# Kernel optimization log

Measured on AMD Instinct MI355X. Metric: run time of the kernel, lower is better.

The kernel has to match this reference:

```python
import jax, jax.numpy as jnp
import numpy as np

N_HEAD, D_K, D_V, D_MODEL, D_O = 8, 64, 64, 512, 512
B, S = 2, 4096

def setup_inputs() -> dict:
    key = jax.random.key(0)
    ks = jax.random.split(key, 11)
    s = 1.0 / np.sqrt(D_MODEL)
    so = 1.0 / np.sqrt(N_HEAD * D_V)
    return {
        'q': jax.random.normal(ks[0], (B, S, D_MODEL), jnp.float32),
        'k': jax.random.normal(ks[1], (B, S, D_MODEL), jnp.float32),
        'v': jax.random.normal(ks[2], (B, S, D_MODEL), jnp.float32),
        'Wq': jax.random.uniform(ks[3], (D_MODEL, N_HEAD * D_K), jnp.float32, -s, s),
        'bq': jax.random.uniform(ks[4], (N_HEAD * D_K,), jnp.float32, -s, s),
        'Wk': jax.random.uniform(ks[5], (D_MODEL, N_HEAD * D_K), jnp.float32, -s, s),
        'bk': jax.random.uniform(ks[6], (N_HEAD * D_K,), jnp.float32, -s, s),
        'Wv': jax.random.uniform(ks[7], (D_MODEL, N_HEAD * D_V), jnp.float32, -s, s),
        'bv': jax.random.uniform(ks[8], (N_HEAD * D_V,), jnp.float32, -s, s),
        'Wo': jax.random.uniform(ks[9], (N_HEAD * D_V, D_O), jnp.float32, -so, so),
        'bo': jax.random.uniform(ks[10], (D_O,), jnp.float32, -so, so),
    }

def reference(q, k, v, Wq, bq, Wk, bk, Wv, bv, Wo, bo):
    b, nq, _ = q.shape
    nk = k.shape[1]
    scale = jnp.asarray(np.power(D_K, 0.5), q.dtype)
    # project and split heads: [b, s, h, d]
    qh = (q @ Wq + bq).reshape(b, nq, N_HEAD, D_K)
    kh = (k @ Wk + bk).reshape(b, nk, N_HEAD, D_K)
    vh = (v @ Wv + bv).reshape(b, nk, N_HEAD, D_V)
    # scaled dot-product attention (full score matrix, as in original)
    scores = jnp.einsum('bqhd,bkhd->bhqk', qh, kh) / scale
    attn = jax.nn.softmax(scores, axis=-1)
    out = jnp.einsum('bhqk,bkhd->bqhd', attn, vh)
    # concat heads (head-major over d_v, matching the original view) and output proj
    out = out.reshape(b, nq, N_HEAD * D_V)
    return out @ Wo + bo
```

## Files before the change

kernel.cpp:

```cpp
#include <hip/hip_runtime.h>
#include <hip/hip_bf16.h>

#define NHEAD 8
#define DK_ 64
#define DM_ 512
#define S_LEN 4096
#define NTOK 8192

typedef __bf16 bf16x8 __attribute__((ext_vector_type(8)));
typedef float f32x4 __attribute__((ext_vector_type(4)));
typedef float f32x16 __attribute__((ext_vector_type(16)));
typedef unsigned int uint4v __attribute__((ext_vector_type(4)));

__device__ __forceinline__ unsigned short f2bf(float f) {
    union { float f; unsigned u; } x; x.f = f;
    unsigned u = x.u;
    u += 0x7FFFu + ((u >> 16) & 1u);
    return (unsigned short)(u >> 16);
}

#if __has_builtin(__builtin_amdgcn_cvt_pk_bf16_f32)
__device__ __forceinline__ unsigned int pkbf(float a, float b) {
    auto r = __builtin_amdgcn_cvt_pk_bf16_f32(a, b);
    unsigned int u; __builtin_memcpy(&u, &r, 4); return u;
}
#else
__device__ __forceinline__ unsigned int pkbf(float a, float b) {
    return (unsigned)f2bf(a) | ((unsigned)f2bf(b) << 16);
}
#endif

#if __has_builtin(__builtin_amdgcn_exp2f)
#define EXP2F(x) __builtin_amdgcn_exp2f(x)
#else
#define EXP2F(x) exp2f(x)
#endif

#if __has_builtin(__builtin_amdgcn_permlane32_swap)
__device__ __forceinline__ void pl32swap(unsigned int& a, unsigned int& b) {
    auto r = __builtin_amdgcn_permlane32_swap(a, b, false, false);
    a = r[0]; b = r[1];
}
#else
__device__ __forceinline__ void pl32swap(unsigned int& a, unsigned int& b) {
    int lane = threadIdx.x & 63;
    unsigned int ax = __shfl_xor((int)a, 32, 64);
    unsigned int bx = __shfl_xor((int)b, 32, 64);
    unsigned int na = (lane < 32) ? a : bx;
    unsigned int nb = (lane < 32) ? ax : b;
    a = na; b = nb;
}
#endif

#define GLOAD_LDS16(gptr, ldsbase) \
    __builtin_amdgcn_global_load_lds((const __attribute__((address_space(1))) unsigned int*)(gptr), \
                                     (__attribute__((address_space(3))) unsigned int*)(ldsbase), 16, 0, 0)

__global__ __launch_bounds__(256) void xcvt(const float* __restrict__ q, const float* __restrict__ k,
                                            const float* __restrict__ v, unsigned short* __restrict__ Xbf) {
    int z = blockIdx.y;
    const float* X = (z == 0) ? q : (z == 1) ? k : v;
    size_t off = (size_t)blockIdx.x * 1024 + threadIdx.x * 4;
    float4 val = *(const float4*)&X[off];
    uint2 o; o.x = pkbf(val.x, val.y); o.y = pkbf(val.z, val.w);
    *(uint2*)&Xbf[(size_t)z * NTOK * DM_ + off] = o;
}

__global__ __launch_bounds__(256) void wtrans(const float* __restrict__ Wq, const float* __restrict__ Wk,
                                              const float* __restrict__ Wv, const float* __restrict__ Wo,
                                              unsigned short* __restrict__ Wt) {
    int z = blockIdx.z;
    const float* W = (z == 0) ? Wq : (z == 1) ? Wk : (z == 2) ? Wv : Wo;
    unsigned short* out = Wt + (size_t)z * DM_ * DM_;
    __shared__ float t[64][65];
    int bn = blockIdx.x * 64, bk = blockIdx.y * 64;
    int tid = threadIdx.x;
    int r0 = tid >> 4, c4 = (tid & 15) * 4;
#pragma unroll
    for (int i = 0; i < 4; i++) {
        int r = r0 + i * 16;
        float4 v = *(const float4*)&W[(size_t)(bk + r) * DM_ + bn + c4];
        t[r][c4] = v.x; t[r][c4 + 1] = v.y; t[r][c4 + 2] = v.z; t[r][c4 + 3] = v.w;
    }
    __syncthreads();
    int n0 = tid >> 4, k4 = (tid & 15) * 4;
#pragma unroll
    for (int i = 0; i < 4; i++) {
        int n = n0 + i * 16;
        ushort4 o;
        o.x = f2bf(t[k4 + 0][n]); o.y = f2bf(t[k4 + 1][n]);
        o.z = f2bf(t[k4 + 2][n]); o.w = f2bf(t[k4 + 3][n]);
        *(ushort4*)&out[(size_t)(bn + n) * DM_ + bk + k4] = o;
    }
}

__device__ __forceinline__ void proj_epilogue(int z, f32x4 (&acc)[4][4], const float* bias,
                                              unsigned short* out, float scale,
                                              int m0, int n0, int mb, int nb, int ln, int qd) {
    float bvv[4];
#pragma unroll
    for (int nt = 0; nt < 4; nt++) bvv[nt] = bias[n0 + nb + nt * 16 + ln];
#pragma unroll
    for (int mt = 0; mt < 4; mt++) {
        int mrow0 = m0 + mb + mt * 16 + qd * 4;
        int b = mrow0 >> 12, s = mrow0 & 4095;
#pragma unroll
        for (int nt = 0; nt < 4; nt++) {
            int ncol = n0 + nb + nt * 16 + ln;
            int h = ncol >> 6, d = ncol & 63;
            if (z == 2) {
                uint2 o;
                o.x = pkbf((acc[mt][nt][0] + bvv[nt]) * scale, (acc[mt][nt][1] + bvv[nt]) * scale);
                o.y = pkbf((acc[mt][nt][2] + bvv[nt]) * scale, (acc[mt][nt][3] + bvv[nt]) * scale);
                *(uint2*)&out[((size_t)(b * NHEAD + h) * DK_ + d) * S_LEN + s] = o;
            } else {
#pragma unroll
                for (int r = 0; r < 4; r++)
                    out[((size_t)(b * NHEAD + h) * S_LEN + (s + r)) * DK_ + d] =
                        f2bf((acc[mt][nt][r] + bvv[nt]) * scale);
            }
        }
    }
}

__global__ __launch_bounds__(256, 3) void qkv_bf(const unsigned short* __restrict__ Xbf,
                                                 const unsigned short* __restrict__ Wt,
                                                 const float* __restrict__ bq, const float* __restrict__ bk,
                                                 const float* __restrict__ bv,
                                                 unsigned short* __restrict__ Qh, unsigned short* __restrict__ Kh,
                                                 unsigned short* __restrict__ VhT) {
    int z = blockIdx.z;
    const unsigned short* X = Xbf + (size_t)z * NTOK * DM_;
    const unsigned short* W = Wt + (size_t)z * DM_ * DM_;
    const float* bias = (z == 0) ? bq : (z == 1) ? bk : bv;
    unsigned short* out = (z == 0) ? Qh : (z == 1) ? Kh : VhT;
    float scale = (z == 0) ? 0.125f * 1.44269504f : 1.0f;

    __shared__ unsigned short As[128 * 40];
    __shared__ unsigned short Bs[128 * 40];
    int tid = threadIdx.x;
    int n0 = blockIdx.x * 128, m0 = blockIdx.y * 128;
    int w = tid >> 6, lane = tid & 63;
    int ln = lane & 15, qd = lane >> 4;
    int mb = (w >> 1) * 64, nb = (w & 1) * 64;

    f32x4 acc[4][4];
#pragma unroll
    for (int i = 0; i < 4; i++)
#pragma unroll
        for (int j = 0; j < 4; j++) { f32x4 zz = {0.f, 0.f, 0.f, 0.f}; acc[i][j] = zz; }

    for (int kk = 0; kk < DM_; kk += 32) {
        __syncthreads();
#pragma unroll
        for (int i = 0; i < 2; i++) {
            int idx = i * 256 + tid;
            int row = idx >> 2, k8 = (idx & 3) * 8;
            uint4 va = *(const uint4*)&X[(size_t)(m0 + row) * DM_ + kk + k8];
            *(uint4*)&As[row * 40 + k8] = va;
            uint4 vb = *(const uint4*)&W[(size_t)(n0 + row) * DM_ + kk + k8];
            *(uint4*)&Bs[row * 40 + k8] = vb;
        }
        __syncthreads();
        bf16x8 af[4], bf[4];
#pragma unroll
        for (int mt = 0; mt < 4; mt++) af[mt] = *(const bf16x8*)&As[(mb + mt * 16 + ln) * 40 + qd * 8];
#pragma unroll
        for (int nt = 0; nt < 4; nt++) bf[nt] = *(const bf16x8*)&Bs[(nb + nt * 16 + ln) * 40 + qd * 8];
#pragma unroll
        for (int mt = 0; mt < 4; mt++)
#pragma unroll
            for (int nt = 0; nt < 4; nt++)
                acc[mt][nt] = __builtin_amdgcn_mfma_f32_16x16x32_bf16(af[mt], bf[nt], acc[mt][nt], 0, 0, 0);
    }
    proj_epilogue(z, acc, bias, out, scale, m0, n0, mb, nb, ln, qd);
}

__global__ __launch_bounds__(256, 3) void qkv_proj(const float* __restrict__ xq, const float* __restrict__ xk,
                                                   const float* __restrict__ xv, const unsigned short* __restrict__ Wt,
                                                   const float* __restrict__ bq, const float* __restrict__ bk,
                                                   const float* __restrict__ bv,
                                                   unsigned short* __restrict__ Qh, unsigned short* __restrict__ Kh,
                                                   unsigned short* __restrict__ VhT) {
    int z = blockIdx.z;
    const float* X = (z == 0) ? xq : (z == 1) ? xk : xv;
    const unsigned short* W = Wt + (size_t)z * DM_ * DM_;
    const float* bias = (z == 0) ? bq : (z == 1) ? bk : bv;
    unsigned short* out = (z == 0) ? Qh : (z == 1) ? Kh : VhT;
    float scale = (z == 0) ? 0.125f * 1.44269504f : 1.0f;

    __shared__ unsigned short As[128 * 40];
    __shared__ unsigned short Bs[128 * 40];
    int tid = threadIdx.x;
    int n0 = blockIdx.x * 128, m0 = blockIdx.y * 128;
    int w = tid >> 6, lane = tid & 63;
    int ln = lane & 15, qd = lane >> 4;
    int mb = (w >> 1) * 64, nb = (w & 1) * 64;

    f32x4 acc[4][4];
#pragma unroll
    for (int i = 0; i < 4; i++)
#pragma unroll
        for (int j = 0; j < 4; j++) { f32x4 zz = {0.f, 0.f, 0.f, 0.f}; acc[i][j] = zz; }

    for (int kk = 0; kk < DM_; kk += 32) {
        __syncthreads();
#pragma unroll
        for (int i = 0; i < 4; i++) {
            int idx = i * 256 + tid;
            int row = idx >> 3, k4 = (idx & 7) * 4;
            float4 v = *(const float4*)&X[(size_t)(m0 + row) * DM_ + kk + k4];
            uint2 o; o.x = pkbf(v.x, v.y); o.y = pkbf(v.z, v.w);
            *(uint2*)&As[row * 40 + k4] = o;
        }
#pragma unroll
        for (int i = 0; i < 2; i++) {
            int idx = i * 256 + tid;
            int row = idx >> 2, k8 = (idx & 3) * 8;
            uint4 v = *(const uint4*)&W[(size_t)(n0 + row) * DM_ + kk + k8];
            *(uint4*)&Bs[row * 40 + k8] = v;
        }
        __syncthreads();
        bf16x8 af[4], bf[4];
#pragma unroll
        for (int mt = 0; mt < 4; mt++) af[mt] = *(const bf16x8*)&As[(mb + mt * 16 + ln) * 40 + qd * 8];
#pragma unroll
        for (int nt = 0; nt < 4; nt++) bf[nt] = *(const bf16x8*)&Bs[(nb + nt * 16 + ln) * 40 + qd * 8];
#pragma unroll
        for (int mt = 0; mt < 4; mt++)
#pragma unroll
            for (int nt = 0; nt < 4; nt++)
                acc[mt][nt] = __builtin_amdgcn_mfma_f32_16x16x32_bf16(af[mt], bf[nt], acc[mt][nt], 0, 0, 0);
    }
    proj_epilogue(z, acc, bias, out, scale, m0, n0, mb, nb, ln, qd);
}

__global__ __launch_bounds__(256, 2) void flash_attn(const unsigned short* __restrict__ Qh,
                                                     const unsigned short* __restrict__ Kh,
                                                     const unsigned short* __restrict__ VhT,
                                                     unsigned short* __restrict__ Ao) {
    __shared__ unsigned short Ks[2][64 * 64];
    __shared__ unsigned short Vs[2][64 * 64];
    int i = blockIdx.x;
    int bh = (i & 7) + 8 * ((i >> 3) & 1);
    int qb = i >> 4;
    int tid = threadIdx.x;
    int w = tid >> 6, lane = tid & 63;
    int ln = lane & 31, hf = lane >> 5;
    int swz = ln & 7;
    int q0 = qb * 128 + w * 32;
    const unsigned short* Qp = Qh + (size_t)bh * S_LEN * DK_;
    const unsigned short* Kp = Kh + (size_t)bh * S_LEN * DK_;
    const unsigned short* Vp = VhT + (size_t)bh * DK_ * S_LEN;

    int sr = lane >> 3;
    int sc = (lane & 7) ^ sr;
    const unsigned short* ksrc = Kp + (size_t)(w * 16 + sr) * DK_ + sc * 8;
    const unsigned short* vsrc = Vp + (size_t)(w * 16 + sr) * S_LEN + sc * 8;

    bf16x8 qf[4];
#pragma unroll
    for (int s = 0; s < 4; s++)
        qf[s] = *(const bf16x8*)&Qp[(size_t)(q0 + ln) * DK_ + s * 16 + hf * 8];

    f32x16 oacc[2];
    { f32x16 z = {0.f}; oacc[0] = z; oacc[1] = z; }
    float lsum = 0.f;

    GLOAD_LDS16(ksrc, &Ks[0][w * 1024]);
    GLOAD_LDS16(ksrc + (size_t)8 * DK_, &Ks[0][w * 1024 + 512]);
    GLOAD_LDS16(vsrc, &Vs[0][w * 1024]);
    GLOAD_LDS16(vsrc + (size_t)8 * S_LEN, &Vs[0][w * 1024 + 512]);

    int p = 0;
    for (int ks = 0; ks < S_LEN; ks += 64, p ^= 1) {
        __syncthreads();
        if (ks + 64 < S_LEN) {
            const unsigned short* kn = ksrc + (size_t)(ks + 64) * DK_;
            const unsigned short* vn = vsrc + (ks + 64);
            GLOAD_LDS16(kn, &Ks[p ^ 1][w * 1024]);
            GLOAD_LDS16(kn + (size_t)8 * DK_, &Ks[p ^ 1][w * 1024 + 512]);
            GLOAD_LDS16(vn, &Vs[p ^ 1][w * 1024]);
            GLOAD_LDS16(vn + (size_t)8 * S_LEN, &Vs[p ^ 1][w * 1024 + 512]);
        }
        const unsigned short* KsT = &Ks[p][0];
        const unsigned short* VsT = &Vs[p][0];

#pragma unroll
        for (int kb = 0; kb < 2; kb++) {
            f32x16 st = {0.f};
#pragma unroll
            for (int s = 0; s < 4; s++) {
                bf16x8 kf = *(const bf16x8*)&KsT[(kb * 32 + ln) * 64 + ((2 * s + hf) ^ swz) * 8];
                st = __builtin_amdgcn_mfma_f32_32x32x16_bf16(kf, qf[s], st, 0, 0, 0);
            }
            float e[16];
#pragma unroll
            for (int r = 0; r < 16; r++) e[r] = EXP2F(st[r]);
            lsum += ((e[0] + e[1]) + (e[2] + e[3])) + ((e[4] + e[5]) + (e[6] + e[7]))
                  + ((e[8] + e[9]) + (e[10] + e[11])) + ((e[12] + e[13]) + (e[14] + e[15]));
            unsigned int g[8];
#pragma unroll
            for (int gi = 0; gi < 8; gi++) g[gi] = pkbf(e[2 * gi], e[2 * gi + 1]);
            pl32swap(g[0], g[2]); pl32swap(g[1], g[3]);
            pl32swap(g[4], g[6]); pl32swap(g[5], g[7]);
            bf16x8 b0, b1;
            { uint4v t = {g[0], g[1], g[2], g[3]}; __builtin_memcpy(&b0, &t, 16); }
            { uint4v t = {g[4], g[5], g[6], g[7]}; __builtin_memcpy(&b1, &t, 16); }
#pragma unroll
            for (int dt = 0; dt < 2; dt++) {
                int s0 = kb * 2;
                bf16x8 vf0 = *(const bf16x8*)&VsT[(dt * 32 + ln) * 64 + ((2 * s0 + hf) ^ swz) * 8];
                bf16x8 vf1 = *(const bf16x8*)&VsT[(dt * 32 + ln) * 64 + ((2 * s0 + 2 + hf) ^ swz) * 8];
                oacc[dt] = __builtin_amdgcn_mfma_f32_32x32x16_bf16(vf0, b0, oacc[dt], 0, 0, 0);
                oacc[dt] = __builtin_amdgcn_mfma_f32_32x32x16_bf16(vf1, b1, oacc[dt], 0, 0, 0);
            }
        }
    }

    float ltot = lsum + __shfl_xor(lsum, 32, 64);
    float inv = 1.0f / ltot;

    int bb = bh >> 3, hh = bh & 7;
    int token = bb * S_LEN + q0 + ln;
#pragma unroll
    for (int dt = 0; dt < 2; dt++)
#pragma unroll
        for (int gi = 0; gi < 8; gi++) {
            int d = dt * 32 + 2 * (gi & 1) + 8 * (gi >> 1) + 4 * hf;
            unsigned int o = pkbf(oacc[dt][2 * gi] * inv, oacc[dt][2 * gi + 1] * inv);
            *(unsigned int*)&Ao[(size_t)token * DM_ + hh * DK_ + d] = o;
        }
}

__global__ __launch_bounds__(256) void out_gemm(const unsigned short* __restrict__ A,
                                                const unsigned short* __restrict__ Wt,
                                                const float* __restrict__ bias, float* __restrict__ out) {
    __shared__ unsigned short As[128 * 40];
    __shared__ unsigned short Bs[128 * 40];
    int tid = threadIdx.x;
    int n0 = blockIdx.x * 128, m0 = blockIdx.y * 128;
    int w = tid >> 6, lane = tid & 63;
    int ln = lane & 15, qd = lane >> 4;
    int mb = (w >> 1) * 64, nb = (w & 1) * 64;

    f32x4 acc[4][4];
#pragma unroll
    for (int i = 0; i < 4; i++)
#pragma unroll
        for (int j = 0; j < 4; j++) { f32x4 z = {0.f, 0.f, 0.f, 0.f}; acc[i][j] = z; }

    for (int kk = 0; kk < DM_; kk += 32) {
        __syncthreads();
#pragma unroll
        for (int i = 0; i < 2; i++) {
            int idx = i * 256 + tid;
            int row = idx >> 2, k8 = (idx & 3) * 8;
            uint4 va = *(const uint4*)&A[(size_t)(m0 + row) * DM_ + kk + k8];
            *(uint4*)&As[row * 40 + k8] = va;
            uint4 vb = *(const uint4*)&Wt[(size_t)(n0 + row) * DM_ + kk + k8];
            *(uint4*)&Bs[row * 40 + k8] = vb;
        }
        __syncthreads();
        bf16x8 af[4], bf[4];
#pragma unroll
        for (int mt = 0; mt < 4; mt++) af[mt] = *(const bf16x8*)&As[(mb + mt * 16 + ln) * 40 + qd * 8];
#pragma unroll
        for (int nt = 0; nt < 4; nt++) bf[nt] = *(const bf16x8*)&Bs[(nb + nt * 16 + ln) * 40 + qd * 8];
#pragma unroll
        for (int mt = 0; mt < 4; mt++)
#pragma unroll
            for (int nt = 0; nt < 4; nt++)
                acc[mt][nt] = __builtin_amdgcn_mfma_f32_16x16x32_bf16(af[mt], bf[nt], acc[mt][nt], 0, 0, 0);
    }

    float bv[4];
#pragma unroll
    for (int nt = 0; nt < 4; nt++) bv[nt] = bias[n0 + nb + nt * 16 + ln];
#pragma unroll
    for (int mt = 0; mt < 4; mt++) {
        int mrow0 = m0 + mb + mt * 16 + qd * 4;
#pragma unroll
        for (int nt = 0; nt < 4; nt++) {
            int ncol = n0 + nb + nt * 16 + ln;
#pragma unroll
            for (int r = 0; r < 4; r++)
                out[(size_t)(mrow0 + r) * DM_ + ncol] = acc[mt][nt][r] + bv[nt];
        }
    }
}

extern "C" void kernel_launch(void* const* d_in, const int* in_sizes, int n_in,
                              void* d_out, int out_size, void* d_ws, size_t ws_size,
                              hipStream_t stream) {
    const float* q  = (const float*)d_in[0];
    const float* k  = (const float*)d_in[1];
    const float* v  = (const float*)d_in[2];
    const float* Wq = (const float*)d_in[3];
    const float* bq = (const float*)d_in[4];
    const float* Wk = (const float*)d_in[5];
    const float* bk = (const float*)d_in[6];
    const float* Wv = (const float*)d_in[7];
    const float* bv = (const float*)d_in[8];
    const float* Wo = (const float*)d_in[9];
    const float* bo = (const float*)d_in[10];
    float* out = (float*)d_out;

    unsigned short* Wt  = (unsigned short*)d_ws;
    unsigned short* Qh  = Wt + (size_t)4 * DM_ * DM_;
    unsigned short* Kh  = Qh + (size_t)NTOK * DM_;
    unsigned short* VhT = Kh + (size_t)NTOK * DM_;
    unsigned short* tail = VhT + (size_t)NTOK * DM_;

    size_t need_bf = ((size_t)4 * DM_ * DM_ + (size_t)6 * NTOK * DM_) * 2;

    wtrans<<<dim3(8, 8, 4), 256, 0, stream>>>(Wq, Wk, Wv, Wo, Wt);
    unsigned short* Ao = tail;
    if (ws_size >= need_bf) {
        unsigned short* Xbf = tail;
        xcvt<<<dim3(4096, 3), 256, 0, stream>>>(q, k, v, Xbf);
        qkv_bf<<<dim3(4, 64, 3), 256, 0, stream>>>(Xbf, Wt, bq, bk, bv, Qh, Kh, VhT);
    } else {
        qkv_proj<<<dim3(4, 64, 3), 256, 0, stream>>>(q, k, v, Wt, bq, bk, bv, Qh, Kh, VhT);
    }
    flash_attn<<<dim3(512), 256, 0, stream>>>(Qh, Kh, VhT, Ao);
    out_gemm<<<dim3(4, 64), 256, 0, stream>>>(Ao, Wt + (size_t)3 * DM_ * DM_, bo, out);
}
```

Measured before the change: 237.7 us.

## Merge prep kernels and use direct-to-LDS swizzled loads in projection GEMMs

```diff
diff --git a/kernel.cpp b/kernel.cpp
--- a/kernel.cpp
+++ b/kernel.cpp
@@ -36,61 +36,52 @@
 #define EXP2F(x) exp2f(x)
 #endif
 
-#if __has_builtin(__builtin_amdgcn_permlane32_swap)
 __device__ __forceinline__ void pl32swap(unsigned int& a, unsigned int& b) {
-    auto r = __builtin_amdgcn_permlane32_swap(a, b, false, false);
-    a = r[0]; b = r[1];
-}
-#else
-__device__ __forceinline__ void pl32swap(unsigned int& a, unsigned int& b) {
-    int lane = threadIdx.x & 63;
-    unsigned int ax = __shfl_xor((int)a, 32, 64);
-    unsigned int bx = __shfl_xor((int)b, 32, 64);
-    unsigned int na = (lane < 32) ? a : bx;
-    unsigned int nb = (lane < 32) ? ax : b;
-    a = na; b = nb;
-}
-#endif
+    asm volatile("v_permlane32_swap_b32 %0, %1" : "+v"(a), "+v"(b));
+}
 
 #define GLOAD_LDS16(gptr, ldsbase) \
     __builtin_amdgcn_global_load_lds((const __attribute__((address_space(1))) unsigned int*)(gptr), \
                                      (__attribute__((address_space(3))) unsigned int*)(ldsbase), 16, 0, 0)
 
-__global__ __launch_bounds__(256) void xcvt(const float* __restrict__ q, const float* __restrict__ k,
-                                            const float* __restrict__ v, unsigned short* __restrict__ Xbf) {
-    int z = blockIdx.y;
-    const float* X = (z == 0) ? q : (z == 1) ? k : v;
-    size_t off = (size_t)blockIdx.x * 1024 + threadIdx.x * 4;
-    float4 val = *(const float4*)&X[off];
-    uint2 o; o.x = pkbf(val.x, val.y); o.y = pkbf(val.z, val.w);
-    *(uint2*)&Xbf[(size_t)z * NTOK * DM_ + off] = o;
-}
-
-__global__ __launch_bounds__(256) void wtrans(const float* __restrict__ Wq, const float* __restrict__ Wk,
-                                              const float* __restrict__ Wv, const float* __restrict__ Wo,
-                                              unsigned short* __restrict__ Wt) {
-    int z = blockIdx.z;
-    const float* W = (z == 0) ? Wq : (z == 1) ? Wk : (z == 2) ? Wv : Wo;
-    unsigned short* out = Wt + (size_t)z * DM_ * DM_;
-    __shared__ float t[64][65];
-    int bn = blockIdx.x * 64, bk = blockIdx.y * 64;
+__global__ __launch_bounds__(256) void prep(const float* __restrict__ q, const float* __restrict__ k,
+                                            const float* __restrict__ v,
+                                            const float* __restrict__ Wq, const float* __restrict__ Wk,
+                                            const float* __restrict__ Wv, const float* __restrict__ Wo,
+                                            unsigned short* __restrict__ Wt, unsigned short* __restrict__ Xbf) {
+    int bid = blockIdx.x;
     int tid = threadIdx.x;
-    int r0 = tid >> 4, c4 = (tid & 15) * 4;
-#pragma unroll
-    for (int i = 0; i < 4; i++) {
-        int r = r0 + i * 16;
-        float4 v = *(const float4*)&W[(size_t)(bk + r) * DM_ + bn + c4];
-        t[r][c4] = v.x; t[r][c4 + 1] = v.y; t[r][c4 + 2] = v.z; t[r][c4 + 3] = v.w;
-    }
-    __syncthreads();
-    int n0 = tid >> 4, k4 = (tid & 15) * 4;
-#pragma unroll
-    for (int i = 0; i < 4; i++) {
-        int n = n0 + i * 16;
-        ushort4 o;
-        o.x = f2bf(t[k4 + 0][n]); o.y = f2bf(t[k4 + 1][n]);
-        o.z = f2bf(t[k4 + 2][n]); o.w = f2bf(t[k4 + 3][n]);
-        *(ushort4*)&out[(size_t)(bn + n) * DM_ + bk + k4] = o;
+    if (bid < 256) {
+        int z = bid >> 6, rem = bid & 63;
+        const float* W = (z == 0) ? Wq : (z == 1) ? Wk : (z == 2) ? Wv : Wo;
+        unsigned short* out = Wt + (size_t)z * DM_ * DM_;
+        __shared__ float t[64][65];
+        int bn = (rem & 7) * 64, bk = (rem >> 3) * 64;
+        int r0 = tid >> 4, c4 = (tid & 15) * 4;
+#pragma unroll
+        for (int i = 0; i < 4; i++) {
+            int r = r0 + i * 16;
+            float4 val = *(const float4*)&W[(size_t)(bk + r) * DM_ + bn + c4];
+            t[r][c4] = val.x; t[r][c4 + 1] = val.y; t[r][c4 + 2] = val.z; t[r][c4 + 3] = val.w;
+        }
+        __syncthreads();
+        int n0 = tid >> 4, k4 = (tid & 15) * 4;
+#pragma unroll
+        for (int i = 0; i < 4; i++) {
+            int n = n0 + i * 16;
+            ushort4 o;
+            o.x = f2bf(t[k4 + 0][n]); o.y = f2bf(t[k4 + 1][n]);
+            o.z = f2bf(t[k4 + 2][n]); o.w = f2bf(t[k4 + 3][n]);
+            *(ushort4*)&out[(size_t)(bn + n) * DM_ + bk + k4] = o;
+        }
+    } else {
+        int tt = bid - 256;
+        int z = tt >> 12, xb = tt & 4095;
+        const float* X = (z == 0) ? q : (z == 1) ? k : v;
+        size_t off = (size_t)xb * 1024 + tid * 4;
+        float4 val = *(const float4*)&X[off];
+        uint2 o; o.x = pkbf(val.x, val.y); o.y = pkbf(val.z, val.w);
+        *(uint2*)&Xbf[(size_t)z * NTOK * DM_ + off] = o;
     }
 }
 
@@ -123,12 +114,59 @@
     }
 }
 
-__global__ __launch_bounds__(256, 3) void qkv_bf(const unsigned short* __restrict__ Xbf,
-                                                 const unsigned short* __restrict__ Wt,
-                                                 const float* __restrict__ bq, const float* __restrict__ bk,
-                                                 const float* __restrict__ bv,
-                                                 unsigned short* __restrict__ Qh, unsigned short* __restrict__ Kh,
-                                                 unsigned short* __restrict__ VhT) {
+__device__ __forceinline__ void gemm_core(const unsigned short* __restrict__ A,
+                                          const unsigned short* __restrict__ B,
+                                          unsigned short* As, unsigned short* Bs,
+                                          int m0, int n0, f32x4 (&acc)[4][4]) {
+    int tid = threadIdx.x;
+    int w = tid >> 6, lane = tid & 63;
+    int ln = lane & 15, qd = lane >> 4;
+    int mb = (w >> 1) * 64, nb = (w & 1) * 64;
+    int sr = lane >> 3;
+    int sc8 = (lane & 7) ^ sr;
+    const unsigned short* asrc = A + (size_t)(m0 + w * 32 + sr) * DM_ + sc8 * 8;
+    const unsigned short* bsrc = B + (size_t)(n0 + w * 32 + sr) * DM_ + sc8 * 8;
+    unsigned short* adst = As + w * 32 * 64;
+    unsigned short* bdst = Bs + w * 32 * 64;
+
+    for (int kk = 0; kk < DM_; kk += 64) {
+        __syncthreads();
+#pragma unroll
+        for (int j = 0; j < 4; j++) {
+            GLOAD_LDS16(asrc + kk + (size_t)(j * 8) * DM_, adst + j * 8 * 64);
+            GLOAD_LDS16(bsrc + kk + (size_t)(j * 8) * DM_, bdst + j * 8 * 64);
+        }
+        __syncthreads();
+#pragma unroll
+        for (int k2 = 0; k2 < 2; k2++) {
+            bf16x8 af[4], bf[4];
+#pragma unroll
+            for (int mt = 0; mt < 4; mt++) {
+                int m = mb + mt * 16 + ln;
+                af[mt] = *(const bf16x8*)&As[m * 64 + ((k2 * 4 + qd) ^ (m & 7)) * 8];
+            }
+#pragma unroll
+            for (int nt = 0; nt < 4; nt++) {
+                int n = nb + nt * 16 + ln;
+                bf[nt] = *(const bf16x8*)&Bs[n * 64 + ((k2 * 4 + qd) ^ (n & 7)) * 8];
+            }
+#pragma unroll
+            for (int mt = 0; mt < 4; mt++)
+#pragma unroll
+                for (int nt = 0; nt < 4; nt++)
+                    acc[mt][nt] = __builtin_amdgcn_mfma_f32_16x16x32_bf16(af[mt], bf[nt], acc[mt][nt], 0, 0, 0);
+        }
+    }
+}
+
+__global__ __launch_bounds__(256) void qkv_bf(const unsigned short* __restrict__ Xbf,
+                                              const unsigned short* __restrict__ Wt,
+                                              const float* __restrict__ bq, const float* __restrict__ bk,
+                                              const float* __restrict__ bv,
+                                              unsigned short* __restrict__ Qh, unsigned short* __restrict__ Kh,
+                                              unsigned short* __restrict__ VhT) {
+    __shared__ unsigned short As[128 * 64];
+    __shared__ unsigned short Bs[128 * 64];
     int z = blockIdx.z;
     const unsigned short* X = Xbf + (size_t)z * NTOK * DM_;
     const unsigned short* W = Wt + (size_t)z * DM_ * DM_;
@@ -136,44 +174,17 @@
     unsigned short* out = (z == 0) ? Qh : (z == 1) ? Kh : VhT;
     float scale = (z == 0) ? 0.125f * 1.44269504f : 1.0f;
 
-    __shared__ unsigned short As[128 * 40];
-    __shared__ unsigned short Bs[128 * 40];
-    int tid = threadIdx.x;
     int n0 = blockIdx.x * 128, m0 = blockIdx.y * 128;
-    int w = tid >> 6, lane = tid & 63;
-    int ln = lane & 15, qd = lane >> 4;
-    int mb = (w >> 1) * 64, nb = (w & 1) * 64;
-
     f32x4 acc[4][4];
 #pragma unroll
     for (int i = 0; i < 4; i++)
 #pragma unroll
         for (int j = 0; j < 4; j++) { f32x4 zz = {0.f, 0.f, 0.f, 0.f}; acc[i][j] = zz; }
 
-    for (int kk = 0; kk < DM_; kk += 32) {
-        __syncthreads();
-#pragma unroll
-        for (int i = 0; i < 2; i++) {
-            int idx = i * 256 + tid;
-            int row = idx >> 2, k8 = (idx & 3) * 8;
-            uint4 va = *(const uint4*)&X[(size_t)(m0 + row) * DM_ + kk + k8];
-            *(uint4*)&As[row * 40 + k8] = va;
-            uint4 vb = *(const uint4*)&W[(size_t)(n0 + row) * DM_ + kk + k8];
-            *(uint4*)&Bs[row * 40 + k8] = vb;
-        }
-        __syncthreads();
-        bf16x8 af[4], bf[4];
-#pragma unroll
-        for (int mt = 0; mt < 4; mt++) af[mt] = *(const bf16x8*)&As[(mb + mt * 16 + ln) * 40 + qd * 8];
-#pragma unroll
-        for (int nt = 0; nt < 4; nt++) bf[nt] = *(const bf16x8*)&Bs[(nb + nt * 16 + ln) * 40 + qd * 8];
-#pragma unroll
-        for (int mt = 0; mt < 4; mt++)
-#pragma unroll
-            for (int nt = 0; nt < 4; nt++)
-                acc[mt][nt] = __builtin_amdgcn_mfma_f32_16x16x32_bf16(af[mt], bf[nt], acc[mt][nt], 0, 0, 0);
-    }
-    proj_epilogue(z, acc, bias, out, scale, m0, n0, mb, nb, ln, qd);
+    gemm_core(X, W, As, Bs, m0, n0, acc);
+
+    int lane = threadIdx.x & 63, w = threadIdx.x >> 6;
+    proj_epilogue(z, acc, bias, out, scale, m0, n0, (w >> 1) * 64, (w & 1) * 64, lane & 15, lane >> 4);
 }
 
 __global__ __launch_bounds__(256, 3) void qkv_proj(const float* __restrict__ xq, const float* __restrict__ xk,
@@ -209,16 +220,16 @@
         for (int i = 0; i < 4; i++) {
             int idx = i * 256 + tid;
             int row = idx >> 3, k4 = (idx & 7) * 4;
-            float4 v = *(const float4*)&X[(size_t)(m0 + row) * DM_ + kk + k4];
-            uint2 o; o.x = pkbf(v.x, v.y); o.y = pkbf(v.z, v.w);
+            float4 val = *(const float4*)&X[(size_t)(m0 + row) * DM_ + kk + k4];
+            uint2 o; o.x = pkbf(val.x, val.y); o.y = pkbf(val.z, val.w);
             *(uint2*)&As[row * 40 + k4] = o;
         }
 #pragma unroll
         for (int i = 0; i < 2; i++) {
             int idx = i * 256 + tid;
             int row = idx >> 2, k8 = (idx & 3) * 8;
-            uint4 v = *(const uint4*)&W[(size_t)(n0 + row) * DM_ + kk + k8];
-            *(uint4*)&Bs[row * 40 + k8] = v;
+            uint4 val = *(const uint4*)&W[(size_t)(n0 + row) * DM_ + kk + k8];
+            *(uint4*)&Bs[row * 40 + k8] = val;
         }
         __syncthreads();
         bf16x8 af[4], bf[4];
@@ -336,44 +347,21 @@
 __global__ __launch_bounds__(256) void out_gemm(const unsigned short* __restrict__ A,
                                                 const unsigned short* __restrict__ Wt,
                                                 const float* __restrict__ bias, float* __restrict__ out) {
-    __shared__ unsigned short As[128 * 40];
-    __shared__ unsigned short Bs[128 * 40];
+    __shared__ unsigned short As[128 * 64];
+    __shared__ unsigned short Bs[128 * 64];
+    int n0 = blockIdx.x * 128, m0 = blockIdx.y * 128;
+    f32x4 acc[4][4];
+#pragma unroll
+    for (int i = 0; i < 4; i++)
+#pragma unroll
+        for (int j = 0; j < 4; j++) { f32x4 z = {0.f, 0.f, 0.f, 0.f}; acc[i][j] = z; }
+
+    gemm_core(A, Wt, As, Bs, m0, n0, acc);
+
     int tid = threadIdx.x;
-    int n0 = blockIdx.x * 128, m0 = blockIdx.y * 128;
     int w = tid >> 6, lane = tid & 63;
     int ln = lane & 15, qd = lane >> 4;
     int mb = (w >> 1) * 64, nb = (w & 1) * 64;
-
-    f32x4 acc[4][4];
-#pragma unroll
-    for (int i = 0; i < 4; i++)
-#pragma unroll
-        for (int j = 0; j < 4; j++) { f32x4 z = {0.f, 0.f, 0.f, 0.f}; acc[i][j] = z; }
-
-    for (int kk = 0; kk < DM_; kk += 32) {
-        __syncthreads();
-#pragma unroll
-        for (int i = 0; i < 2; i++) {
-            int idx = i * 256 + tid;
-            int row = idx >> 2, k8 = (idx & 3) * 8;
-            uint4 va = *(const uint4*)&A[(size_t)(m0 + row) * DM_ + kk + k8];
-            *(uint4*)&As[row * 40 + k8] = va;
-            uint4 vb = *(const uint4*)&Wt[(size_t)(n0 + row) * DM_ + kk + k8];
-            *(uint4*)&Bs[row * 40 + k8] = vb;
-        }
-        __syncthreads();
-        bf16x8 af[4], bf[4];
-#pragma unroll
-        for (int mt = 0; mt < 4; mt++) af[mt] = *(const bf16x8*)&As[(mb + mt * 16 + ln) * 40 + qd * 8];
-#pragma unroll
-        for (int nt = 0; nt < 4; nt++) bf[nt] = *(const bf16x8*)&Bs[(nb + nt * 16 + ln) * 40 + qd * 8];
-#pragma unroll
-        for (int mt = 0; mt < 4; mt++)
-#pragma unroll
-            for (int nt = 0; nt < 4; nt++)
-                acc[mt][nt] = __builtin_amdgcn_mfma_f32_16x16x32_bf16(af[mt], bf[nt], acc[mt][nt], 0, 0, 0);
-    }
-
     float bv[4];
 #pragma unroll
     for (int nt = 0; nt < 4; nt++) bv[nt] = bias[n0 + nb + nt * 16 + ln];
@@ -413,14 +401,15 @@
     unsigned short* tail = VhT + (size_t)NTOK * DM_;
 
     size_t need_bf = ((size_t)4 * DM_ * DM_ + (size_t)6 * NTOK * DM_) * 2;
-
-    wtrans<<<dim3(8, 8, 4), 256, 0, stream>>>(Wq, Wk, Wv, Wo, Wt);
+    bool use_bf = ws_size >= need_bf;
+
     unsigned short* Ao = tail;
-    if (ws_size >= need_bf) {
+    if (use_bf) {
         unsigned short* Xbf = tail;
-        xcvt<<<dim3(4096, 3), 256, 0, stream>>>(q, k, v, Xbf);
+        prep<<<dim3(256 + 3 * 4096), 256, 0, stream>>>(q, k, v, Wq, Wk, Wv, Wo, Wt, Xbf);
         qkv_bf<<<dim3(4, 64, 3), 256, 0, stream>>>(Xbf, Wt, bq, bk, bv, Qh, Kh, VhT);
     } else {
+        prep<<<dim3(256), 256, 0, stream>>>(q, k, v, Wq, Wk, Wv, Wo, Wt, nullptr);
         qkv_proj<<<dim3(4, 64, 3), 256, 0, stream>>>(q, k, v, Wt, bq, bk, bv, Qh, Kh, VhT);
     }
     flash_attn<<<dim3(512), 256, 0, stream>>>(Qh, Kh, VhT, Ao);
```

Measured after the change: 243.2 us. +2.3%, slower.
